# Kernel tuning notes

Measured on AMD Instinct MI355X. Metric: run time of the kernel, lower is better.

Reference implementation:

```python
import jax, jax.numpy as jnp
import numpy as np

N_NODES = 200000
IN_SIZE = 128
OUT_SIZE = 128
N_EDGES = 600000


def setup_inputs() -> dict:
    key = jax.random.key(0)
    k1, k2, k3, k4 = jax.random.split(key, 4)
    embedding = jax.random.normal(k1, (N_NODES, IN_SIZE), dtype=jnp.float32)
    up2down_edge_index = jax.random.randint(k2, (2, N_EDGES), 0, N_NODES, dtype=jnp.int64)
    # GCNConv params (glorot weight, zero bias as in PyG defaults)
    scale = np.sqrt(6.0 / (IN_SIZE + OUT_SIZE)).astype(np.float32)
    W = jax.random.uniform(k3, (IN_SIZE, OUT_SIZE), dtype=jnp.float32, minval=-scale, maxval=scale)
    b = jnp.zeros((OUT_SIZE,), dtype=jnp.float32)
    return {"embedding": embedding, "up2down_edge_index": up2down_edge_index, "W": W, "b": b}


def reference(embedding, up2down_edge_index, W, b):
    # PyG GCNConv: add self-loops, symmetric normalization, linear transform,
    # scatter-sum aggregation, add bias.
    N = embedding.shape[0]
    loops = jnp.arange(N, dtype=up2down_edge_index.dtype)
    src = jnp.concatenate([up2down_edge_index[0], loops])  # message sources
    dst = jnp.concatenate([up2down_edge_index[1], loops])  # message targets

    # degree of each target node (edge_weight = 1)
    deg = jax.ops.segment_sum(jnp.ones_like(src, dtype=embedding.dtype), dst, num_segments=N)
    deg_inv_sqrt = jnp.where(deg > 0, jax.lax.rsqrt(jnp.maximum(deg, 1.0)), 0.0)
    norm = deg_inv_sqrt[src] * deg_inv_sqrt[dst]  # [E+N]

    h = embedding @ W  # [N, out]
    msg = h[src] * norm[:, None]  # gather + scale, [E+N, out]
    out = jax.ops.segment_sum(msg, dst, num_segments=N)  # scatter-add
    return out + b
```

## Files before the change

### kernel.cpp

```cpp
#include <hip/hip_runtime.h>
#include <hip/hip_bf16.h>
#include <stdint.h>

typedef __attribute__((ext_vector_type(8))) short short8v;
typedef __attribute__((ext_vector_type(4))) float f32x4;

__device__ __forceinline__ unsigned short f2bf(float f) {
  unsigned int u = __float_as_uint(f);
  u += 0x7fffu + ((u >> 16) & 1u);
  return (unsigned short)(u >> 16);
}
__device__ __forceinline__ unsigned int pack2bf(float a, float b) {
  return (unsigned int)f2bf(a) | ((unsigned int)f2bf(b) << 16);
}
__device__ __forceinline__ float bf_lo(unsigned int v) { return __uint_as_float(v << 16); }
__device__ __forceinline__ float bf_hi(unsigned int v) { return __uint_as_float(v & 0xffff0000u); }

__global__ void k_prep(uint4* __restrict__ zp, int n16,
                       const float* __restrict__ W, unsigned short* __restrict__ Wfrag) {
  int b = blockIdx.x;
  if (b < 64) {
    int t = b * 256 + threadIdx.x;
    int j = t & 7;
    int lane = (t >> 3) & 63;
    int ktct = t >> 9;
    int kt = ktct & 3, ct = ktct >> 2;
    int col = ct * 16 + (lane & 15);
    int k = kt * 32 + 4 * (lane >> 4) + (j & 3) + 16 * (j >> 2);
    Wfrag[t] = f2bf(W[k * 128 + col]);
  } else {
    int i = (b - 64) * 256 + threadIdx.x;
    if (i < n16) {
      uint4 z; z.x = z.y = z.z = z.w = 0u;
      zp[i] = z;
    }
  }
}

__global__ void k_count(const int* __restrict__ dst, int* deg, int E) {
  int e = blockIdx.x * blockDim.x + threadIdx.x;
  if (e < E) atomicAdd(&deg[dst[e]], 1);
}

__global__ void k_blocksum(const int* __restrict__ deg, int* partials, float* dis, int N) {
  __shared__ int s[256];
  int t = threadIdx.x;
  int i = blockIdx.x * 256 + t;
  int c = (i < N) ? deg[i] : 0;
  if (i < N) dis[i] = rsqrtf((float)(c + 1));
  s[t] = c;
  __syncthreads();
  for (int off = 128; off > 0; off >>= 1) {
    if (t < off) s[t] += s[t + off];
    __syncthreads();
  }
  if (t == 0) partials[blockIdx.x] = s[0];
}

__global__ void k_scan_final2(const int* __restrict__ deg, const int* __restrict__ partials,
                              int* csr_off, int N, int E) {
  __shared__ int s[256];
  __shared__ int base;
  int t = threadIdx.x;
  int accp = 0;
  for (int j = t; j < blockIdx.x; j += 256) accp += partials[j];
  s[t] = accp;
  __syncthreads();
  for (int off = 128; off > 0; off >>= 1) {
    if (t < off) s[t] += s[t + off];
    __syncthreads();
  }
  if (t == 0) base = s[0];
  __syncthreads();
  int i = blockIdx.x * 256 + t;
  int c = (i < N) ? deg[i] : 0;
  s[t] = c;
  __syncthreads();
  for (int off = 1; off < 256; off <<= 1) {
    int v = (t >= off) ? s[t - off] : 0;
    __syncthreads();
    s[t] += v;
    __syncthreads();
  }
  if (i < N) csr_off[i] = base + s[t] - c;
  if (i == 0) csr_off[N] = E;
}

__global__ void k_fill(const int* __restrict__ src, const int* __restrict__ dst,
                       const int* __restrict__ csr_off, int* cursor, int* csr_src, int E) {
  int e = blockIdx.x * blockDim.x + threadIdx.x;
  if (e < E) {
    int d = dst[e];
    int p = atomicAdd(&cursor[d], 1);
    csr_src[csr_off[d] + p] = src[e];
  }
}

__device__ __forceinline__ short8v pack8(f32x4 a, f32x4 b) {
  short8v r;
  r[0] = (short)f2bf(a[0]); r[1] = (short)f2bf(a[1]);
  r[2] = (short)f2bf(a[2]); r[3] = (short)f2bf(a[3]);
  r[4] = (short)f2bf(b[0]); r[5] = (short)f2bf(b[1]);
  r[6] = (short)f2bf(b[2]); r[7] = (short)f2bf(b[3]);
  return r;
}


#define GLOAD(XB, DD, TT, HAS)                                                  \
  do {                                                                          \
    if (HAS) {                                                                  \
      int row_ = (TT) * 16 + lr;                                                \
      if (row_ < N) {                                                           \
        const float* xp_ = X + (size_t)row_ * 128 + 4 * lg;                     \
        _Pragma("unroll") for (int q = 0; q < 4; ++q) {                         \
          XB[2 * q]     = __builtin_nontemporal_load((const f32x4*)(xp_ + q * 32));      \
          XB[2 * q + 1] = __builtin_nontemporal_load((const f32x4*)(xp_ + q * 32 + 16)); \
        }                                                                       \
        DD = dis[row_];                                                         \
      } else {                                                                  \
        _Pragma("unroll") for (int q = 0; q < 8; ++q) {                         \
          XB[q][0] = XB[q][1] = XB[q][2] = XB[q][3] = 0.f;                      \
        }                                                                       \
        DD = 0.f;                                                               \
      }                                                                         \
    }                                                                           \
  } while (0)

#define GCOMPUTE(XB, DD, TT)                                                    \
  do {                                                                          \
    short8v afr[4];                                                             \
    _Pragma("unroll") for (int kt = 0; kt < 4; ++kt)                            \
        afr[kt] = pack8(XB[2 * kt], XB[2 * kt + 1]);                            \
    int row_ = (TT) * 16 + lr;                                                  \
    bool wr_ = row_ < N;                                                        \
    unsigned short* hp_ = hs + (size_t)row_ * 128;                              \
    float dd_ = DD;                                                             \
    _Pragma("unroll") for (int cp = 0; cp < 4; ++cp) {                          \
      f32x4 a0 = {0.f, 0.f, 0.f, 0.f}, a1 = {0.f, 0.f, 0.f, 0.f};               \
      _Pragma("unroll") for (int kt = 0; kt < 4; ++kt)                          \
          a0 = __builtin_amdgcn_mfma_f32_16x16x32_bf16(wreg[(2 * cp) * 4 + kt], \
                                                       afr[kt], a0, 0, 0, 0);   \
      _Pragma("unroll") for (int kt = 0; kt < 4; ++kt)                          \
          a1 = __builtin_amdgcn_mfma_f32_16x16x32_bf16(                         \
              wreg[(2 * cp + 1) * 4 + kt], afr[kt], a1, 0, 0, 0);               \
      unsigned int u0x = pack2bf(a0[0] * dd_, a0[1] * dd_);                     \
      unsigned int u0y = pack2bf(a0[2] * dd_, a0[3] * dd_);                     \
      unsigned int u1x = pack2bf(a1[0] * dd_, a1[1] * dd_);                     \
      unsigned int u1y = pack2bf(a1[2] * dd_, a1[3] * dd_);                     \
      int s_ = lg & 1;                                                          \
      unsigned int sx = s_ ? u0x : u1x, sy = s_ ? u0y : u1y;                    \
      unsigned int rx = (unsigned int)__shfl_xor((int)sx, 16);                  \
      unsigned int ry = (unsigned int)__shfl_xor((int)sy, 16);                  \
      uint4 uu;                                                                 \
      if (s_ == 0) { uu.x = u0x; uu.y = u0y; uu.z = rx; uu.w = ry; }            \
      else         { uu.x = rx; uu.y = ry; uu.z = u1x; uu.w = u1y; }            \
      int cb = (s_ ? (2 * cp + 1) : (2 * cp)) * 16 + 8 * (lg >> 1);             \
      if (wr_) *(uint4*)(hp_ + cb) = uu;                                        \
    }                                                                           \
  } while (0)

__global__ __launch_bounds__(256, 2) void k_gemm5(const float* __restrict__ X,
     const unsigned short* __restrict__ Wfrag, const float* __restrict__ dis,
     unsigned short* __restrict__ hs, int N, int ntile) {
  int lane = threadIdx.x & 63;
  int gw = (blockIdx.x * blockDim.x + threadIdx.x) >> 6;
  int nw = (gridDim.x * blockDim.x) >> 6;
  int lr = lane & 15, lg = lane >> 4;

  short8v wreg[32];
  #pragma unroll
  for (int f = 0; f < 32; ++f)
    wreg[f] = *(const short8v*)(Wfrag + (size_t)(f * 64 + lane) * 8);

  int tile = gw;
  if (tile >= ntile) return;

  f32x4 xv[8], nx[8];
  float d0 = 0.f, d1 = 0.f;
  GLOAD(xv, d0, tile, true);

  for (;;) {
    int t1 = tile + nw;
    bool h1 = t1 < ntile;
    GLOAD(nx, d1, t1, h1);
    GCOMPUTE(xv, d0, tile);
    if (!h1) break;
    int t2 = t1 + nw;
    bool h2 = t2 < ntile;
    GLOAD(xv, d0, t2, h2);
    GCOMPUTE(nx, d1, t1);
    if (!h2) break;
    tile = t2;
  }
}

__device__ __forceinline__ void acc8(float* a, uint4 g) {
  a[0] += bf_lo(g.x); a[1] += bf_hi(g.x);
  a[2] += bf_lo(g.y); a[3] += bf_hi(g.y);
  a[4] += bf_lo(g.z); a[5] += bf_hi(g.z);
  a[6] += bf_lo(g.w); a[7] += bf_hi(g.w);
}

__global__ __launch_bounds__(256) void k_agg2(const unsigned short* __restrict__ hs_,
     const int* __restrict__ csr_src, const int* __restrict__ csr_off,
     const float* __restrict__ dis, const float* __restrict__ bias,
     float* __restrict__ out, int N) {
  const uint4* hs = (const uint4*)hs_;
  int lane = threadIdx.x & 63;
  int c = lane & 15;
  int base = lane & 48;
  int gid = (blockIdx.x * blockDim.x + threadIdx.x) >> 4;
  int G = (gridDim.x * blockDim.x) >> 4;
  int i0 = (int)(((long long)gid * N) / G);
  int i1 = (int)(((long long)(gid + 1) * N) / G);
  if (i0 >= i1) return;
  float4 bA = ((const float4*)bias)[c * 2];
  float4 bB = ((const float4*)bias)[c * 2 + 1];
  int e1prev = csr_off[i0];
  for (int i = i0; i < i1; ++i) {
    int e0 = e1prev;
    int e1 = csr_off[i + 1];
    e1prev = e1;
    float a[8];
    uint4 sv = hs[(size_t)i * 16 + c];
    a[0] = bf_lo(sv.x); a[1] = bf_hi(sv.x);
    a[2] = bf_lo(sv.y); a[3] = bf_hi(sv.y);
    a[4] = bf_lo(sv.z); a[5] = bf_hi(sv.z);
    a[6] = bf_lo(sv.w); a[7] = bf_hi(sv.w);
    int e = e0;
    while (e < e1) {
      int p = e + c;
      int myidx = (p < e1) ? csr_src[p] : 0;
      int kb = (e1 - e < 16) ? (e1 - e) : 16;
      int k = 0;
      for (; k + 8 <= kb; k += 8) {
        int s[8];
        #pragma unroll
        for (int q = 0; q < 8; ++q) s[q] = __shfl(myidx, base + k + q);
        uint4 g[8];
        #pragma unroll
        for (int q = 0; q < 8; ++q) g[q] = hs[(size_t)s[q] * 16 + c];
        #pragma unroll
        for (int q = 0; q < 8; ++q) acc8(a, g[q]);
      }
      for (; k < kb; k += 4) {
        int s0 = __shfl(myidx, base + k);
        int s1 = __shfl(myidx, base + k + 1);
        int s2 = __shfl(myidx, base + k + 2);
        int s3 = __shfl(myidx, base + k + 3);
        bool v1 = (k + 1 < kb), v2 = (k + 2 < kb), v3 = (k + 3 < kb);
        uint4 g0 = hs[(size_t)s0 * 16 + c];
        uint4 g1 = hs[(size_t)(v1 ? s1 : i) * 16 + c];
        uint4 g2 = hs[(size_t)(v2 ? s2 : i) * 16 + c];
        uint4 g3 = hs[(size_t)(v3 ? s3 : i) * 16 + c];
        if (!v1) { g1.x = g1.y = g1.z = g1.w = 0u; }
        if (!v2) { g2.x = g2.y = g2.z = g2.w = 0u; }
        if (!v3) { g3.x = g3.y = g3.z = g3.w = 0u; }
        acc8(a, g0); acc8(a, g1); acc8(a, g2); acc8(a, g3);
      }
      e += kb;
    }
    float di = dis[i];
    f32x4 o0, o1;
    o0[0] = fmaf(di, a[0], bA.x); o0[1] = fmaf(di, a[1], bA.y);
    o0[2] = fmaf(di, a[2], bA.z); o0[3] = fmaf(di, a[3], bA.w);
    o1[0] = fmaf(di, a[4], bB.x); o1[1] = fmaf(di, a[5], bB.y);
    o1[2] = fmaf(di, a[6], bB.z); o1[3] = fmaf(di, a[7], bB.w);
    f32x4* op = (f32x4*)(out + (size_t)i * 128);
    __builtin_nontemporal_store(o0, op + c * 2);
    __builtin_nontemporal_store(o1, op + c * 2 + 1);
  }
}

extern "C" void kernel_launch(void* const* d_in, const int* in_sizes, int n_in,
                              void* d_out, int out_size, void* d_ws, size_t ws_size,
                              hipStream_t stream) {
  const float* X    = (const float*)d_in[0];
  const int*   edge = (const int*)d_in[1];
  const float* W    = (const float*)d_in[2];
  const float* bias = (const float*)d_in[3];
  float* out = (float*)d_out;
  int N = in_sizes[0] / 128;
  int E = in_sizes[1] / 2;
  const int* srcArr = edge;
  const int* dstArr = edge + E;

  char* w = (char*)d_ws;
  auto align = [](size_t x) { return (x + 255) & ~(size_t)255; };
  size_t o = 0;
  int*   deg      = (int*)(w + o);   o += align((size_t)N * 4);
  int*   cursor   = (int*)(w + o);   o += align((size_t)N * 4);
  float* dis      = (float*)(w + o); o += align((size_t)N * 4);
  int*   csr_off  = (int*)(w + o);   o += align(((size_t)N + 1) * 4);
  int*   csr_src  = (int*)(w + o);   o += align((size_t)E * 4);
  int*   partials = (int*)(w + o);   o += align((size_t)4096 * 4);
  unsigned short* Wfrag = (unsigned short*)(w + o); o += align((size_t)16384 * 2);
  unsigned short* hs    = (unsigned short*)(w + o);

  int nbN = (N + 255) / 256;
  int nbE = (E + 255) / 256;
  int ntile = (N + 15) / 16;

  size_t zbytes = align((size_t)N * 4) + align((size_t)N * 4);
  int n16 = (int)(zbytes / 16);
  k_prep<<<64 + (n16 + 255) / 256, 256, 0, stream>>>((uint4*)deg, n16, W, Wfrag);
  k_count<<<nbE, 256, 0, stream>>>(dstArr, deg, E);
  k_blocksum<<<nbN, 256, 0, stream>>>(deg, partials, dis, N);
  k_scan_final2<<<nbN, 256, 0, stream>>>(deg, partials, csr_off, N, E);
  k_fill<<<nbE, 256, 0, stream>>>(srcArr, dstArr, csr_off, cursor, csr_src, E);
  k_gemm5<<<512, 256, 0, stream>>>(X, Wfrag, dis, hs, N, ntile);
  k_agg2<<<2048, 256, 0, stream>>>(hs, csr_src, csr_off, dis, bias, out, N);
}
```

Baseline: 160.6 us.

## Fuse CSR construction into one cooperative kernel with grid syncs

Replaces the separate zeroing, degree-count, block-sum, scan and fill kernels with a single cooperative kernel that separates its phases with grid-wide syncs. The degree array doubles as the fill cursor through atomicSub, which removes the separate cursor buffer and its zeroing. The goal is to cut per-launch overhead and the gaps between the small kernels. Two smaller tweaks ride along: the GEMM's X loads become ordinary loads instead of nontemporal ones, and the aggregation grid is doubled. The cost is that all blocks must be co-resident for the cooperative launch, and each grid.sync adds its own expense.

```diff
diff --git a/kernel.cpp b/kernel.cpp
--- a/kernel.cpp
+++ b/kernel.cpp
@@ -1,6 +1,9 @@
 #include <hip/hip_runtime.h>
 #include <hip/hip_bf16.h>
+#include <hip/hip_cooperative_groups.h>
 #include <stdint.h>
+
+namespace cg = cooperative_groups;
 
 typedef __attribute__((ext_vector_type(8))) short short8v;
 typedef __attribute__((ext_vector_type(4))) float f32x4;
@@ -16,36 +19,34 @@
 __device__ __forceinline__ float bf_lo(unsigned int v) { return __uint_as_float(v << 16); }
 __device__ __forceinline__ float bf_hi(unsigned int v) { return __uint_as_float(v & 0xffff0000u); }
 
-__global__ void k_prep(uint4* __restrict__ zp, int n16,
-                       const float* __restrict__ W, unsigned short* __restrict__ Wfrag) {
+__global__ void k_wprep(const float* __restrict__ W, unsigned short* __restrict__ Wfrag) {
+  int t = blockIdx.x * 256 + threadIdx.x;
+  int j = t & 7;
+  int lane = (t >> 3) & 63;
+  int ktct = t >> 9;
+  int kt = ktct & 3, ct = ktct >> 2;
+  int col = ct * 16 + (lane & 15);
+  int k = kt * 32 + 4 * (lane >> 4) + (j & 3) + 16 * (j >> 2);
+  Wfrag[t] = f2bf(W[k * 128 + col]);
+}
+
+__global__ void k_csr(const int* __restrict__ src, const int* __restrict__ dst,
+                      int* __restrict__ deg, float* __restrict__ dis,
+                      int* __restrict__ csr_off, int* __restrict__ partials,
+                      int* __restrict__ csr_src, int N, int E) {
+  cg::grid_group grid = cg::this_grid();
+  __shared__ int s[256];
+  __shared__ int base;
+  int t = threadIdx.x;
   int b = blockIdx.x;
-  if (b < 64) {
-    int t = b * 256 + threadIdx.x;
-    int j = t & 7;
-    int lane = (t >> 3) & 63;
-    int ktct = t >> 9;
-    int kt = ktct & 3, ct = ktct >> 2;
-    int col = ct * 16 + (lane & 15);
-    int k = kt * 32 + 4 * (lane >> 4) + (j & 3) + 16 * (j >> 2);
-    Wfrag[t] = f2bf(W[k * 128 + col]);
-  } else {
-    int i = (b - 64) * 256 + threadIdx.x;
-    if (i < n16) {
-      uint4 z; z.x = z.y = z.z = z.w = 0u;
-      zp[i] = z;
-    }
-  }
-}
-
-__global__ void k_count(const int* __restrict__ dst, int* deg, int E) {
-  int e = blockIdx.x * blockDim.x + threadIdx.x;
-  if (e < E) atomicAdd(&deg[dst[e]], 1);
-}
-
-__global__ void k_blocksum(const int* __restrict__ deg, int* partials, float* dis, int N) {
-  __shared__ int s[256];
-  int t = threadIdx.x;
-  int i = blockIdx.x * 256 + t;
+  int nthr = gridDim.x * 256;
+  int gtid = b * 256 + t;
+
+  for (int i = gtid; i < N; i += nthr) deg[i] = 0;
+  grid.sync();
+  for (int e = gtid; e < E; e += nthr) atomicAdd(&deg[dst[e]], 1);
+  grid.sync();
+  int i = gtid;
   int c = (i < N) ? deg[i] : 0;
   if (i < N) dis[i] = rsqrtf((float)(c + 1));
   s[t] = c;
@@ -54,16 +55,10 @@
     if (t < off) s[t] += s[t + off];
     __syncthreads();
   }
-  if (t == 0) partials[blockIdx.x] = s[0];
-}
-
-__global__ void k_scan_final2(const int* __restrict__ deg, const int* __restrict__ partials,
-                              int* csr_off, int N, int E) {
-  __shared__ int s[256];
-  __shared__ int base;
-  int t = threadIdx.x;
+  if (t == 0) partials[b] = s[0];
+  grid.sync();
   int accp = 0;
-  for (int j = t; j < blockIdx.x; j += 256) accp += partials[j];
+  for (int j = t; j < b; j += 256) accp += partials[j];
   s[t] = accp;
   __syncthreads();
   for (int off = 128; off > 0; off >>= 1) {
@@ -72,8 +67,6 @@
   }
   if (t == 0) base = s[0];
   __syncthreads();
-  int i = blockIdx.x * 256 + t;
-  int c = (i < N) ? deg[i] : 0;
   s[t] = c;
   __syncthreads();
   for (int off = 1; off < 256; off <<= 1) {
@@ -84,14 +77,10 @@
   }
   if (i < N) csr_off[i] = base + s[t] - c;
   if (i == 0) csr_off[N] = E;
-}
-
-__global__ void k_fill(const int* __restrict__ src, const int* __restrict__ dst,
-                       const int* __restrict__ csr_off, int* cursor, int* csr_src, int E) {
-  int e = blockIdx.x * blockDim.x + threadIdx.x;
-  if (e < E) {
+  grid.sync();
+  for (int e = gtid; e < E; e += nthr) {
     int d = dst[e];
-    int p = atomicAdd(&cursor[d], 1);
+    int p = atomicSub(&deg[d], 1) - 1;
     csr_src[csr_off[d] + p] = src[e];
   }
 }
@@ -113,8 +102,8 @@
       if (row_ < N) {                                                           \
         const float* xp_ = X + (size_t)row_ * 128 + 4 * lg;                     \
         _Pragma("unroll") for (int q = 0; q < 4; ++q) {                         \
-          XB[2 * q]     = __builtin_nontemporal_load((const f32x4*)(xp_ + q * 32));      \
-          XB[2 * q + 1] = __builtin_nontemporal_load((const f32x4*)(xp_ + q * 32 + 16)); \
+          XB[2 * q]     = *(const f32x4*)(xp_ + q * 32);                        \
+          XB[2 * q + 1] = *(const f32x4*)(xp_ + q * 32 + 16);                   \
         }                                                                       \
         DD = dis[row_];                                                         \
       } else {                                                                  \
@@ -282,14 +271,13 @@
   float* out = (float*)d_out;
   int N = in_sizes[0] / 128;
   int E = in_sizes[1] / 2;
-  const int* srcArr = edge;
-  const int* dstArr = edge + E;
+  const int* srcArr = (const int*)edge;
+  const int* dstArr = (const int*)(edge + E);
 
   char* w = (char*)d_ws;
   auto align = [](size_t x) { return (x + 255) & ~(size_t)255; };
   size_t o = 0;
   int*   deg      = (int*)(w + o);   o += align((size_t)N * 4);
-  int*   cursor   = (int*)(w + o);   o += align((size_t)N * 4);
   float* dis      = (float*)(w + o); o += align((size_t)N * 4);
   int*   csr_off  = (int*)(w + o);   o += align(((size_t)N + 1) * 4);
   int*   csr_src  = (int*)(w + o);   o += align((size_t)E * 4);
@@ -298,16 +286,16 @@
   unsigned short* hs    = (unsigned short*)(w + o);
 
   int nbN = (N + 255) / 256;
-  int nbE = (E + 255) / 256;
   int ntile = (N + 15) / 16;
 
-  size_t zbytes = align((size_t)N * 4) + align((size_t)N * 4);
-  int n16 = (int)(zbytes / 16);
-  k_prep<<<64 + (n16 + 255) / 256, 256, 0, stream>>>((uint4*)deg, n16, W, Wfrag);
-  k_count<<<nbE, 256, 0, stream>>>(dstArr, deg, E);
-  k_blocksum<<<nbN, 256, 0, stream>>>(deg, partials, dis, N);
-  k_scan_final2<<<nbN, 256, 0, stream>>>(deg, partials, csr_off, N, E);
-  k_fill<<<nbE, 256, 0, stream>>>(srcArr, dstArr, csr_off, cursor, csr_src, E);
+  k_wprep<<<64, 256, 0, stream>>>(W, Wfrag);
+  {
+    void* args[] = { (void*)&srcArr, (void*)&dstArr, (void*)&deg, (void*)&dis,
+                     (void*)&csr_off, (void*)&partials, (void*)&csr_src,
+                     (void*)&N, (void*)&E };
+    hipLaunchCooperativeKernel((const void*)k_csr, dim3(nbN), dim3(256),
+                               args, 0, stream);
+  }
   k_gemm5<<<512, 256, 0, stream>>>(X, Wfrag, dis, hs, N, ntile);
-  k_agg2<<<2048, 256, 0, stream>>>(hs, csr_src, csr_off, dis, bias, out, N);
-}
+  k_agg2<<<4096, 256, 0, stream>>>(hs, csr_src, csr_off, dis, bias, out, N);
+}
```

Measured after the change: 458.8 us. 186% more time.
